# Optimization experiments

Hardware: AMD Instinct MI355X
Metric: run time of the kernel (lower is better)

## Reference

```python
import jax, jax.numpy as jnp
import numpy as np

NUM_CLASSES = 7


def setup_inputs() -> dict:
    key = jax.random.key(0)
    k1, k2, k3, k4 = jax.random.split(key, 4)
    B, C, D = 65536, NUM_CLASSES, 512
    outputs = jax.random.normal(k1, (B, C), dtype=jnp.float32)
    features = jax.random.normal(k2, (B, D), dtype=jnp.float32)
    targets = jax.random.randint(k3, (B,), 0, C, dtype=jnp.int64)
    attention_weights = jax.random.uniform(k4, (B, D), dtype=jnp.float32)
    return {"outputs": outputs, "features": features, "targets": targets,
            "attention_weights": attention_weights}


def reference(outputs, features, targets, attention_weights):
    lambda_val = 0.1
    B = features.shape[0]
    C = outputs.shape[1]

    # Cross-entropy (mean over batch), matching nn.CrossEntropyLoss
    logp = jax.nn.log_softmax(outputs, axis=-1)  # [B, C]
    ce_loss = -jnp.mean(jnp.take_along_axis(logp, targets[:, None], axis=1))

    # Per-class centers via segment reduce (replaces python loop over classes)
    sums = jax.ops.segment_sum(features, targets, num_segments=C)      # [C, D]
    counts = jax.ops.segment_sum(jnp.ones((B,), features.dtype), targets,
                                 num_segments=C)                        # [C]
    present = counts > 0
    centers = sums / jnp.maximum(counts, 1.0)[:, None]                  # [C, D]

    # Squared distance to own-class center (replaces python loop over batch);
    # samples whose class is absent (impossible here, but kept faithful) add 0.
    diff = features - centers[targets]                                  # [B, D]
    per_sample = jnp.sum(diff * diff, axis=-1) * present[targets].astype(features.dtype)
    center_loss = jnp.sum(per_sample) / B

    l1_loss = jnp.mean(jnp.abs(attention_weights))

    total_loss = ce_loss + lambda_val * center_loss + 0.01 * l1_loss
    return (total_loss, ce_loss, center_loss, l1_loss)
```

## Files before the change

### kernel.cpp

```cpp
#include <hip/hip_runtime.h>

static constexpr int BATCH  = 65536;
static constexpr int DDIM   = 512;
static constexpr int NCLS   = 7;
static constexpr int SLICE  = NCLS * DDIM;
static constexpr int SLICEP = SLICE + 16;
static constexpr int NRED   = NCLS * 16;

template <int RPB>
__global__ __launch_bounds__(512, 6) void k_main(const float4* __restrict__ F,
                                                 const float4* __restrict__ A,
                                                 const int* __restrict__ tg,
                                                 const float* __restrict__ outputs,
                                                 float* __restrict__ part) {
  const int tid  = threadIdx.x;
  const int bid  = blockIdx.x;
  const int c4   = tid & 127;
  const int ph   = tid >> 7;
  const int base = bid * RPB;

  float4 acc[NCLS];
#pragma unroll
  for (int c = 0; c < NCLS; ++c) acc[c] = make_float4(0.f, 0.f, 0.f, 0.f);
  float sumsq = 0.f, l1 = 0.f;

#pragma unroll 2
  for (int r = base; r < base + RPB; r += 8) {
    const int4 ta = *reinterpret_cast<const int4*>(tg + r);
    const int4 tb = *reinterpret_cast<const int4*>(tg + r + 4);
    const size_t i0 = (size_t)(r + ph) * 128 + c4;
    const float4 f0 = F[i0];
    const float4 f1 = F[i0 + 512];
    const float4 w0 = A[i0];
    const float4 w1 = A[i0 + 512];
    const int t0 = (ph == 0) ? ta.x : (ph == 1) ? ta.y : (ph == 2) ? ta.z : ta.w;
    const int t1 = (ph == 0) ? tb.x : (ph == 1) ? tb.y : (ph == 2) ? tb.z : tb.w;

    sumsq = fmaf(f0.x, f0.x, sumsq); sumsq = fmaf(f0.y, f0.y, sumsq);
    sumsq = fmaf(f0.z, f0.z, sumsq); sumsq = fmaf(f0.w, f0.w, sumsq);
    sumsq = fmaf(f1.x, f1.x, sumsq); sumsq = fmaf(f1.y, f1.y, sumsq);
    sumsq = fmaf(f1.z, f1.z, sumsq); sumsq = fmaf(f1.w, f1.w, sumsq);
    l1 += fabsf(w0.x) + fabsf(w0.y) + fabsf(w0.z) + fabsf(w0.w) +
          fabsf(w1.x) + fabsf(w1.y) + fabsf(w1.z) + fabsf(w1.w);

#pragma unroll
    for (int c = 0; c < NCLS; ++c) {
      acc[c].x += (t0 == c) ? f0.x : 0.f;
      acc[c].y += (t0 == c) ? f0.y : 0.f;
      acc[c].z += (t0 == c) ? f0.z : 0.f;
      acc[c].w += (t0 == c) ? f0.w : 0.f;
      acc[c].x += (t1 == c) ? f1.x : 0.f;
      acc[c].y += (t1 == c) ? f1.y : 0.f;
      acc[c].z += (t1 == c) ? f1.z : 0.f;
      acc[c].w += (t1 == c) ? f1.w : 0.f;
    }
  }

  __shared__ float red[256][33];
  if (ph >= 2) {
    float* row = red[(ph - 2) * 128 + c4];
#pragma unroll
    for (int c = 0; c < NCLS; ++c) {
      row[c * 4 + 0] = acc[c].x; row[c * 4 + 1] = acc[c].y;
      row[c * 4 + 2] = acc[c].z; row[c * 4 + 3] = acc[c].w;
    }
    row[28] = sumsq; row[29] = l1;
  }
  __syncthreads();
  if (ph < 2) {
    const float* row = red[ph * 128 + c4];
#pragma unroll
    for (int c = 0; c < NCLS; ++c) {
      acc[c].x += row[c * 4 + 0]; acc[c].y += row[c * 4 + 1];
      acc[c].z += row[c * 4 + 2]; acc[c].w += row[c * 4 + 3];
    }
    sumsq += row[28]; l1 += row[29];
  }
  __syncthreads();
  if (ph == 1) {
    float* row = red[c4];
#pragma unroll
    for (int c = 0; c < NCLS; ++c) {
      row[c * 4 + 0] = acc[c].x; row[c * 4 + 1] = acc[c].y;
      row[c * 4 + 2] = acc[c].z; row[c * 4 + 3] = acc[c].w;
    }
    row[28] = sumsq; row[29] = l1;
  }
  __syncthreads();

  __shared__ float s2[2], s3[2];
  if (ph == 0) {
    const float* row = red[c4];
#pragma unroll
    for (int c = 0; c < NCLS; ++c) {
      acc[c].x += row[c * 4 + 0]; acc[c].y += row[c * 4 + 1];
      acc[c].z += row[c * 4 + 2]; acc[c].w += row[c * 4 + 3];
    }
    sumsq += row[28]; l1 += row[29];

    float4* __restrict__ myp = reinterpret_cast<float4*>(part + (size_t)bid * SLICEP);
#pragma unroll
    for (int c = 0; c < NCLS; ++c) myp[c * 128 + c4] = acc[c];

    float bs = sumsq, bl = l1;
#pragma unroll
    for (int off = 32; off > 0; off >>= 1) {
      bs += __shfl_down(bs, off);
      bl += __shfl_down(bl, off);
    }
    if ((tid & 63) == 0) { s2[tid >> 6] = bs; s3[tid >> 6] = bl; }
  }

  constexpr int NACT = (RPB / 64 < 8) ? RPB / 64 : 8;
  __shared__ float ce_w[8];
  __shared__ float cw_w[8][8];
  const int lane = tid & 63, wid = tid >> 6;
  if (wid < NACT) {
    float ce = 0.f;
    float cw[NCLS];
#pragma unroll
    for (int c = 0; c < NCLS; ++c) cw[c] = 0.f;
    for (int r0 = wid * 64; r0 < RPB; r0 += NACT * 64) {
      const int row = base + r0 + lane;
      const float* o = outputs + (size_t)row * NCLS;
      const float x0 = o[0], x1 = o[1], x2 = o[2], x3 = o[3],
                  x4 = o[4], x5 = o[5], x6 = o[6];
      const float m = fmaxf(fmaxf(fmaxf(x0, x1), fmaxf(x2, x3)),
                            fmaxf(fmaxf(x4, x5), x6));
      const float s = expf(x0 - m) + expf(x1 - m) + expf(x2 - m) + expf(x3 - m) +
                      expf(x4 - m) + expf(x5 - m) + expf(x6 - m);
      const int t = tg[row];
      const float xt = (t == 0) ? x0 : (t == 1) ? x1 : (t == 2) ? x2 :
                       (t == 3) ? x3 : (t == 4) ? x4 : (t == 5) ? x5 : x6;
      ce += (m - xt) + logf(s);
#pragma unroll
      for (int c = 0; c < NCLS; ++c)
        cw[c] += (float)__popcll(__ballot(t == c)) * ((lane == 0) ? 1.f : 0.f);
    }
#pragma unroll
    for (int off = 32; off > 0; off >>= 1) ce += __shfl_down(ce, off);
    if (lane == 0) {
      ce_w[wid] = ce;
#pragma unroll
      for (int c = 0; c < NCLS; ++c) cw_w[wid][c] = cw[c];
    }
  }
  __syncthreads();

  if (tid == 0) {
    float ceb = 0.f, cb[NCLS];
#pragma unroll
    for (int c = 0; c < NCLS; ++c) cb[c] = 0.f;
#pragma unroll
    for (int w = 0; w < NACT; ++w) {
      ceb += ce_w[w];
#pragma unroll
      for (int c = 0; c < NCLS; ++c) cb[c] += cw_w[w][c];
    }
    float* sp = part + (size_t)bid * SLICEP + SLICE;
    sp[0] = s2[0] + s2[1];
    sp[1] = s3[0] + s3[1];
    sp[2] = ceb;
#pragma unroll
    for (int c = 0; c < NCLS; ++c) sp[3 + c] = cb[c];
  }
}

__global__ __launch_bounds__(256) void k_reduce(const float* __restrict__ part,
                                                double* __restrict__ qpart,
                                                int nblk) {
  const int c  = blockIdx.x >> 4;
  const int cg = blockIdx.x & 15;
  const int t  = threadIdx.x;
  const int col = cg * 32 + (t & 31);
  const int sl0 = t >> 5;

  float s = 0.f;
#pragma unroll 4
  for (int sl = sl0; sl < nblk; sl += 8)
    s += part[(size_t)sl * SLICEP + c * DDIM + col];

  __shared__ float red[8][33];
  red[sl0][t & 31] = s;
  __syncthreads();

  if (t < 32) {
    float S = 0.f;
#pragma unroll
    for (int i = 0; i < 8; ++i) S += red[i][t];
    float q = S * S;
#pragma unroll
    for (int off = 16; off > 0; off >>= 1) q += __shfl_down(q, off);
    if (t == 0) qpart[blockIdx.x] = (double)q;
  }
}

__global__ __launch_bounds__(512) void k_fin(const float* __restrict__ part,
                                             const double* __restrict__ qpart,
                                             float* __restrict__ out, int nblk) {
  const int t = threadIdx.x;
  const int lane = t & 63, wid = t >> 6;

  double ss = 0.0, l1 = 0.0, ce = 0.0;
  float cnt[NCLS];
#pragma unroll
  for (int c = 0; c < NCLS; ++c) cnt[c] = 0.f;
  for (int sl = t; sl < nblk; sl += 512) {
    const float* sp = part + (size_t)sl * SLICEP + SLICE;
    ss += (double)sp[0];
    l1 += (double)sp[1];
    ce += (double)sp[2];
#pragma unroll
    for (int c = 0; c < NCLS; ++c) cnt[c] += sp[3 + c];
  }

#pragma unroll
  for (int off = 32; off > 0; off >>= 1) {
    ss += __shfl_down(ss, off);
    l1 += __shfl_down(l1, off);
    ce += __shfl_down(ce, off);
#pragma unroll
    for (int c = 0; c < NCLS; ++c) cnt[c] += __shfl_down(cnt[c], off);
  }

  __shared__ double lss[8], ll1[8], lce[8];
  __shared__ float lcnt[8][8];
  if (lane == 0) {
    lss[wid] = ss; ll1[wid] = l1; lce[wid] = ce;
#pragma unroll
    for (int c = 0; c < NCLS; ++c) lcnt[wid][c] = cnt[c];
  }
  __syncthreads();

  __shared__ float counts_sh[NCLS];
  __shared__ double tot[3];
  if (t == 0) {
    double a = 0, b = 0, d = 0;
    float cc[NCLS];
#pragma unroll
    for (int c = 0; c < NCLS; ++c) cc[c] = 0.f;
#pragma unroll
    for (int w = 0; w < 8; ++w) {
      a += lss[w]; b += ll1[w]; d += lce[w];
#pragma unroll
      for (int c = 0; c < NCLS; ++c) cc[c] += lcnt[w][c];
    }
    tot[0] = a; tot[1] = b; tot[2] = d;
#pragma unroll
    for (int c = 0; c < NCLS; ++c) counts_sh[c] = cc[c];
  }
  __syncthreads();

  double myq = 0.0;
  if (t < NRED) {
    const float cn = counts_sh[t >> 4];
    myq = (cn > 0.f) ? qpart[t] / (double)cn : 0.0;
  }
#pragma unroll
  for (int off = 32; off > 0; off >>= 1) myq += __shfl_down(myq, off);
  __shared__ double qs[2];
  if (lane == 0 && wid < 2) qs[wid] = myq;
  __syncthreads();

  if (t == 0) {
    const double wcss = qs[0] + qs[1];
    const double center = (tot[0] - wcss) / (double)BATCH;
    const double cem = tot[2] / (double)BATCH;
    const double l1m = tot[1] / ((double)BATCH * (double)DDIM);
    out[0] = (float)(cem + 0.1 * center + 0.01 * l1m);
    out[1] = (float)cem;
    out[2] = (float)center;
    out[3] = (float)l1m;
  }
}

extern "C" void kernel_launch(void* const* d_in, const int* in_sizes, int n_in,
                              void* d_out, int out_size, void* d_ws, size_t ws_size,
                              hipStream_t stream) {
  const float*  outputs  = (const float*)d_in[0];
  const float4* features = (const float4*)d_in[1];
  const int*    targets  = (const int*)d_in[2];
  const float4* aw       = (const float4*)d_in[3];
  float* out = (float*)d_out;
  float* part = (float*)d_ws;

  auto need = [](int nblk) { return (size_t)nblk * SLICEP * 4 + NRED * 8; };
  int nblk = 128;
  if (ws_size >= need(512)) nblk = 512;
  else if (ws_size >= need(256)) nblk = 256;
  double* qpart = (double*)((char*)d_ws + (size_t)nblk * SLICEP * 4);

  switch (nblk) {
    case 512: k_main<128><<<512, 512, 0, stream>>>(features, aw, targets, outputs, part); break;
    case 256: k_main<256><<<256, 512, 0, stream>>>(features, aw, targets, outputs, part); break;
    default:  k_main<512><<<128, 512, 0, stream>>>(features, aw, targets, outputs, part); break;
  }
  k_reduce<<<NRED, 256, 0, stream>>>(part, qpart, nblk);
  k_fin<<<1, 512, 0, stream>>>(part, qpart, out, nblk);
}
```

Before: 60.77 us.

## Fuse reduce and finalize kernels via last-block atomic; nontemporal attention loads

Merges the per-class reduce kernel and the single-block finalize kernel into one launch: each reduce block bumps an atomic counter after writing its partial, and the last block performs the final reduction with 256 threads instead of 512. A memset of the counter is added to the stream. Attention-weight loads in the main kernel are switched to nontemporal loads, since that data is streamed once. This removes one kernel launch gap at the cost of an extra memset and a serialized tail in the last block.

```diff
diff --git a/kernel.cpp b/kernel.cpp
--- a/kernel.cpp
+++ b/kernel.cpp
@@ -6,6 +6,13 @@
 static constexpr int SLICE  = NCLS * DDIM;
 static constexpr int SLICEP = SLICE + 16;
 static constexpr int NRED   = NCLS * 16;
+
+typedef float f32x4 __attribute__((ext_vector_type(4)));
+
+__device__ __forceinline__ float4 ntload4(const float4* p) {
+  f32x4 v = __builtin_nontemporal_load(reinterpret_cast<const f32x4*>(p));
+  return make_float4(v.x, v.y, v.z, v.w);
+}
 
 template <int RPB>
 __global__ __launch_bounds__(512, 6) void k_main(const float4* __restrict__ F,
@@ -31,8 +38,8 @@
     const size_t i0 = (size_t)(r + ph) * 128 + c4;
     const float4 f0 = F[i0];
     const float4 f1 = F[i0 + 512];
-    const float4 w0 = A[i0];
-    const float4 w1 = A[i0 + 512];
+    const float4 w0 = ntload4(A + i0);
+    const float4 w1 = ntload4(A + i0 + 512);
     const int t0 = (ph == 0) ? ta.x : (ph == 1) ? ta.y : (ph == 2) ? ta.z : ta.w;
     const int t1 = (ph == 0) ? tb.x : (ph == 1) ? tb.y : (ph == 2) ? tb.z : tb.w;
 
@@ -166,9 +173,11 @@
   }
 }
 
-__global__ __launch_bounds__(256) void k_reduce(const float* __restrict__ part,
-                                                double* __restrict__ qpart,
-                                                int nblk) {
+__global__ __launch_bounds__(256) void k_reduce_fin(const float* __restrict__ part,
+                                                    double* __restrict__ qpart,
+                                                    unsigned* __restrict__ done,
+                                                    float* __restrict__ out,
+                                                    int nblk) {
   const int c  = blockIdx.x >> 4;
   const int cg = blockIdx.x & 15;
   const int t  = threadIdx.x;
@@ -193,42 +202,44 @@
     for (int off = 16; off > 0; off >>= 1) q += __shfl_down(q, off);
     if (t == 0) qpart[blockIdx.x] = (double)q;
   }
-}
-
-__global__ __launch_bounds__(512) void k_fin(const float* __restrict__ part,
-                                             const double* __restrict__ qpart,
-                                             float* __restrict__ out, int nblk) {
-  const int t = threadIdx.x;
+
+  __shared__ bool amlast;
+  __syncthreads();
+  if (t == 0) {
+    __threadfence();
+    amlast = (atomicAdd(done, 1u) == NRED - 1);
+  }
+  __syncthreads();
+  if (!amlast) return;
+  __threadfence();
+
   const int lane = t & 63, wid = t >> 6;
-
   double ss = 0.0, l1 = 0.0, ce = 0.0;
   float cnt[NCLS];
 #pragma unroll
-  for (int c = 0; c < NCLS; ++c) cnt[c] = 0.f;
-  for (int sl = t; sl < nblk; sl += 512) {
+  for (int k = 0; k < NCLS; ++k) cnt[k] = 0.f;
+  for (int sl = t; sl < nblk; sl += 256) {
     const float* sp = part + (size_t)sl * SLICEP + SLICE;
     ss += (double)sp[0];
     l1 += (double)sp[1];
     ce += (double)sp[2];
 #pragma unroll
-    for (int c = 0; c < NCLS; ++c) cnt[c] += sp[3 + c];
-  }
-
+    for (int k = 0; k < NCLS; ++k) cnt[k] += sp[3 + k];
+  }
 #pragma unroll
   for (int off = 32; off > 0; off >>= 1) {
     ss += __shfl_down(ss, off);
     l1 += __shfl_down(l1, off);
     ce += __shfl_down(ce, off);
 #pragma unroll
-    for (int c = 0; c < NCLS; ++c) cnt[c] += __shfl_down(cnt[c], off);
-  }
-
-  __shared__ double lss[8], ll1[8], lce[8];
-  __shared__ float lcnt[8][8];
+    for (int k = 0; k < NCLS; ++k) cnt[k] += __shfl_down(cnt[k], off);
+  }
+  __shared__ double lss[4], ll1[4], lce[4];
+  __shared__ float lcnt[4][8];
   if (lane == 0) {
     lss[wid] = ss; ll1[wid] = l1; lce[wid] = ce;
 #pragma unroll
-    for (int c = 0; c < NCLS; ++c) lcnt[wid][c] = cnt[c];
+    for (int k = 0; k < NCLS; ++k) lcnt[wid][k] = cnt[k];
   }
   __syncthreads();
 
@@ -238,16 +249,16 @@
     double a = 0, b = 0, d = 0;
     float cc[NCLS];
 #pragma unroll
-    for (int c = 0; c < NCLS; ++c) cc[c] = 0.f;
-#pragma unroll
-    for (int w = 0; w < 8; ++w) {
+    for (int k = 0; k < NCLS; ++k) cc[k] = 0.f;
+#pragma unroll
+    for (int w = 0; w < 4; ++w) {
       a += lss[w]; b += ll1[w]; d += lce[w];
 #pragma unroll
-      for (int c = 0; c < NCLS; ++c) cc[c] += lcnt[w][c];
+      for (int k = 0; k < NCLS; ++k) cc[k] += lcnt[w][k];
     }
     tot[0] = a; tot[1] = b; tot[2] = d;
 #pragma unroll
-    for (int c = 0; c < NCLS; ++c) counts_sh[c] = cc[c];
+    for (int k = 0; k < NCLS; ++k) counts_sh[k] = cc[k];
   }
   __syncthreads();
 
@@ -284,17 +295,19 @@
   float* out = (float*)d_out;
   float* part = (float*)d_ws;
 
-  auto need = [](int nblk) { return (size_t)nblk * SLICEP * 4 + NRED * 8; };
+  auto need = [](int nblk) { return (size_t)nblk * SLICEP * 4 + NRED * 8 + 4; };
   int nblk = 128;
   if (ws_size >= need(512)) nblk = 512;
   else if (ws_size >= need(256)) nblk = 256;
   double* qpart = (double*)((char*)d_ws + (size_t)nblk * SLICEP * 4);
+  unsigned* done = (unsigned*)((char*)qpart + NRED * 8);
+
+  hipMemsetAsync(done, 0, 4, stream);
 
   switch (nblk) {
     case 512: k_main<128><<<512, 512, 0, stream>>>(features, aw, targets, outputs, part); break;
     case 256: k_main<256><<<256, 512, 0, stream>>>(features, aw, targets, outputs, part); break;
     default:  k_main<512><<<128, 512, 0, stream>>>(features, aw, targets, outputs, part); break;
   }
-  k_reduce<<<NRED, 256, 0, stream>>>(part, qpart, nblk);
-  k_fin<<<1, 512, 0, stream>>>(part, qpart, out, nblk);
+  k_reduce_fin<<<NRED, 256, 0, stream>>>(part, qpart, done, out, nblk);
 }
```

After: 65.50 us. 7.8% more time.
